# Optimization experiments

Measured on AMD Instinct MI355X. Metric: run time of the kernel, lower is better.

The kernel has to match this reference:

```python
import jax, jax.numpy as jnp
import numpy as np

B, S, D = 1, 1024, 1024
NH, DH, DR = 8, 128, 64
DCQ, DC = 768, 256
INTER, E, TOPK = 512, 8, 2

def rmsnorm(x, w, eps=1e-6):
    return x * jax.lax.rsqrt(jnp.mean(x * x, -1, keepdims=True) + eps) * w

def lin(x, w, b):
    return x @ w.T + b

def apply_rope(x, cos, sin):
    # x: [b, s, h, d]; cos/sin: [S, d//2]; complex rotate pairs (even, odd)
    b, s, h, d = x.shape
    xr = x.reshape(b, s, h, d // 2, 2)
    x0, x1 = xr[..., 0], xr[..., 1]
    c = cos[None, :s, None, :]
    sn = sin[None, :s, None, :]
    return jnp.stack([x0 * c - x1 * sn, x0 * sn + x1 * c], -1).reshape(b, s, h, d)

def setup_inputs():
    keys = iter(jax.random.split(jax.random.key(0), 64))
    def nrm(*shape):
        return jax.random.normal(next(keys), shape, jnp.float32) * 0.02
    theta = 1.0 / (10000.0 ** (jnp.arange(0, DR, 2, dtype=jnp.float32) / DR))
    ang = jnp.arange(S, dtype=jnp.float32)[:, None] * theta[None, :]
    return dict(
        h=jax.random.normal(next(keys), (B, S, D), jnp.float32),
        freqs_cos=jnp.cos(ang), freqs_sin=jnp.sin(ang),
        mask=jnp.triu(jnp.ones((S, S), bool), 1),
        attn_norm_w=jnp.ones(D), ffn_norm_w=jnp.ones(D),
        wq_down=nrm(DCQ, D), bq_down=jnp.zeros(DCQ), q_norm_w=jnp.ones(DCQ),
        wqc=nrm(NH * DH, DCQ), bqc=jnp.zeros(NH * DH),
        wqr=nrm(NH * DR, DCQ), bqr=jnp.zeros(NH * DR),
        wkr=nrm(DR, D), bkr=jnp.zeros(DR), kr_norm_w=jnp.ones(DR),
        wkv_down=nrm(DC, D), bkv_down=jnp.zeros(DC), kv_norm_w=jnp.ones(DC),
        wkc=nrm(NH * DH, DC), bkc=jnp.zeros(NH * DH),
        wvc=nrm(NH * DH, DC), bvc=jnp.zeros(NH * DH),
        wo=nrm(D, NH * DH), bo=jnp.zeros(D),
        sw1=nrm(INTER, D), sb1=jnp.zeros(INTER), sw2=nrm(D, INTER), sb2=jnp.zeros(D),
        sw3=nrm(INTER, D), sb3=jnp.zeros(INTER),
        ew1=nrm(E, INTER, D), eb1=jnp.zeros((E, INTER)), ew2=nrm(E, D, INTER), eb2=jnp.zeros((E, D)),
        ew3=nrm(E, INTER, D), eb3=jnp.zeros((E, INTER)),
        centroids=jax.random.normal(next(keys), (E, D), jnp.float32), biases=jnp.zeros(E),
    )

def _forward(h, freqs_cos, freqs_sin, mask, attn_norm_w, ffn_norm_w, wq_down, bq_down, q_norm_w, wqc, bqc, wqr, bqr, wkr, bkr, kr_norm_w, wkv_down, bkv_down, kv_norm_w, wkc, bkc, wvc, bvc, wo, bo, sw1, sb1, sw2, sb2, sw3, sb3, ew1, eb1, ew2, eb2, ew3, eb3, centroids, biases):
    b, s, _ = h.shape
    # --- pre-norm MLA attention ---
    x = rmsnorm(h, attn_norm_w)
    cQ = rmsnorm(lin(x, wq_down, bq_down), q_norm_w)
    qR = apply_rope(lin(cQ, wqr, bqr).reshape(b, s, NH, DR), freqs_cos, freqs_sin)
    qC = lin(cQ, wqc, bqc).reshape(b, s, NH, DH)
    q = jnp.concatenate([qC, qR], -1)                      # [b,s,NH,DH+DR]
    kR = apply_rope(rmsnorm(lin(x, wkr, bkr), kr_norm_w).reshape(b, s, 1, DR), freqs_cos, freqs_sin)
    cKV = rmsnorm(lin(x, wkv_down, bkv_down), kv_norm_w)
    kC = lin(cKV, wkc, bkc).reshape(b, s, NH, DH)
    vC = lin(cKV, wvc, bvc).reshape(b, s, NH, DH)
    k = jnp.concatenate([jnp.broadcast_to(kR, (b, s, NH, DR)), kC], -1)  # source order: [kR, kC]
    scores = jnp.einsum('bqhd,bkhd->bhqk', q, k) / jnp.sqrt(jnp.float32(DH + DR))
    scores = jnp.where(mask[None, None], jnp.finfo(scores.dtype).min, scores)
    attw = jax.nn.softmax(scores, -1)                      # dropout in eval mode = identity
    attn = jnp.einsum('bhqk,bkhd->bqhd', attw, vC).reshape(b, s, NH * DH)
    x1 = h + lin(attn, wo, bo)
    # --- pre-norm MoE FFN ---
    y = rmsnorm(x1, ffn_norm_w)
    shared = lin(jax.nn.silu(lin(y, sw1, sb1)) * lin(y, sw3, sb3), sw2, sb2)  # mean over 1 shared expert
    affinity = jax.nn.sigmoid(y @ centroids.T)             # [b,s,E]
    _, topi = jax.lax.top_k(affinity + biases, TOPK)
    gates = jax.nn.softmax(jnp.take_along_axis(affinity, topi, -1), -1)      # [b,s,TOPK]
    combine = (jax.nn.one_hot(topi, E, dtype=y.dtype) * gates[..., None]).sum(-2)  # [b,s,E]
    h1 = jax.nn.silu(jnp.einsum('bsd,eid->bsei', y, ew1) + eb1) * (jnp.einsum('bsd,eid->bsei', y, ew3) + eb3)
    out_e = jnp.einsum('bsei,edi->bsed', h1, ew2) + eb2
    routed = (out_e * combine[..., None]).sum(2)
    return x1 + shared + routed

def reference(h, freqs_cos, freqs_sin, mask, attn_norm_w, ffn_norm_w, wq_down, bq_down, q_norm_w, wqc, bqc, wqr, bqr, wkr, bkr, kr_norm_w, wkv_down, bkv_down, kv_norm_w, wkc, bkc, wvc, bvc, wo, bo, sw1, sb1, sw2, sb2, sw3, sb3, ew1, eb1, ew2, eb2, ew3, eb3, centroids, biases):
    return _forward(h, freqs_cos, freqs_sin, mask, attn_norm_w, ffn_norm_w, wq_down, bq_down, q_norm_w, wqc, bqc, wqr, bqr, wkr, bkr, kr_norm_w, wkv_down, bkv_down, kv_norm_w, wkc, bkc, wvc, bvc, wo, bo, sw1, sb1, sw2, sb2, sw3, sb3, ew1, eb1, ew2, eb2, ew3, eb3, centroids, biases)
```

## Files before the change

kernel.cpp:

```cpp
#include <hip/hip_runtime.h>

typedef unsigned short u16;
typedef __attribute__((ext_vector_type(8))) short short8;
typedef __attribute__((ext_vector_type(4))) float f32x4;

__device__ __forceinline__ float b2f(u16 u) { return __uint_as_float(((unsigned)u) << 16); }
__device__ __forceinline__ u16 f2b(float f) {
    unsigned x = __float_as_uint(f);
    return (u16)((x + 0x7fffu + ((x >> 16) & 1u)) >> 16);
}

#define GLDS16(gp, lp) __builtin_amdgcn_global_load_lds( \
    (const __attribute__((address_space(1))) void*)(gp), \
    (__attribute__((address_space(3))) void*)(lp), 16, 0, 0)

#define WAITV(N) do { \
    asm volatile("s_waitcnt vmcnt(" #N ")" ::: "memory"); \
    __builtin_amdgcn_sched_barrier(0); \
} while (0)

#define KC8_SWZ(lane) ((((lane) & 3) ^ (((lane) >> 3) & 3)) << 3)
#define RD_SWZ(fm, fq) (((fq) ^ (((fm) >> 1) & 3)) << 3)

__device__ __forceinline__ void xcd_swz(int& bx, int& by) {
    if ((gridDim.x & 7) == 0 && gridDim.y == 16) {
        int lid = bx + by * gridDim.x;
        int q = lid >> 3, r = lid & 7;
        by = q & 15;
        bx = r + ((q >> 4) << 3);
    }
}

struct Seg { const u16* W; const float* bias; void* C; int ldc; int epi; int bx0; int aidx; };
struct GArgs {
    const u16* A[2]; int lda[2]; int K[2];
    Seg seg[4]; int nseg;
    const float* res;
    float* dst2;
};

__launch_bounds__(256)
__global__ void mgemm4(GArgs ga)
{
    __shared__ u16 As[6 * 2048];
    __shared__ u16 Bs[6 * 2048];
    int bx = blockIdx.x, by = blockIdx.y;
    xcd_swz(bx, by);
    int si = 0;
#pragma unroll
    for (int i = 1; i < 4; i++)
        if (i < ga.nseg && bx >= ga.seg[i].bx0) si = i;
    const u16* Wp = ga.seg[si].W;
    const float* bp = ga.seg[si].bias;
    void* Cp = ga.seg[si].C;
    const int ldco = ga.seg[si].ldc;
    const int epi = ga.seg[si].epi;
    const int ai = ga.seg[si].aidx;
    const u16* Ap = ga.A[ai];
    const int lda = ga.lda[ai], K = ga.K[ai];
    const int col0 = (bx - ga.seg[si].bx0) * 64;
    const int row0 = by * 64;

    int tid = threadIdx.x;
    int lane = tid & 63, w = tid >> 6;
    int r0 = (w << 4) + (lane >> 2), kc8 = KC8_SWZ(lane);
    const u16* gA = Ap + (size_t)(row0 + r0) * lda + kc8;
    const u16* gB = Wp + (size_t)(col0 + r0) * lda + kc8;

    int fm = lane & 15, fq = lane >> 4;
    const int so = RD_SWZ(fm, fq);
    f32x4 acc[4] = {};

#define MG_STAGE(BS, KO) do { \
    GLDS16(gA + (KO), As + (BS) * 2048 + (w << 9)); \
    GLDS16(gB + (KO), Bs + (BS) * 2048 + (w << 9)); \
} while (0)

    const int nst = K >> 5;
    MG_STAGE(0, 0); MG_STAGE(1, 32); MG_STAGE(2, 64); MG_STAGE(3, 96);
    int bcur = 0;
    for (int t = 0; t < nst; t += 2) {
        if (t < nst - 2) { WAITV(4); } else { WAITV(0); }
        __builtin_amdgcn_s_barrier();
        int w4 = bcur + 4; if (w4 >= 6) w4 -= 6;
        int w5 = w4 + 1;   if (w5 >= 6) w5 -= 6;
        if (t + 4 < nst) MG_STAGE(w4, (t + 4) << 5);
        if (t + 5 < nst) MG_STAGE(w5, (t + 5) << 5);
#pragma unroll
        for (int sub = 0; sub < 2; sub++) {
            int bc = bcur + sub; if (bc >= 6) bc -= 6;
            short8 af = *(const short8*)(As + bc * 2048 + (w << 9) + fm * 32 + so);
            short8 bf[4];
#pragma unroll
            for (int nt = 0; nt < 4; nt++)
                bf[nt] = *(const short8*)(Bs + bc * 2048 + ((nt << 4) + fm) * 32 + so);
#pragma unroll
            for (int nt = 0; nt < 4; nt++)
                acc[nt] = __builtin_amdgcn_mfma_f32_16x16x32_bf16(af, bf[nt], acc[nt], 0, 0, 0);
        }
        bcur += 2; if (bcur >= 6) bcur -= 6;
    }
#undef MG_STAGE

    int rbase = row0 + (w << 4) + (fq << 2);
#pragma unroll
    for (int nt = 0; nt < 4; nt++) {
        int c = col0 + (nt << 4) + fm;
        float bcol = bp[c];
#pragma unroll
        for (int reg = 0; reg < 4; reg++) {
            int r = rbase + reg;
            float v = acc[nt][reg] + bcol;
            if (epi == 3)
                ((u16*)Cp)[(size_t)r * ldco + c] = f2b(v);
            else if (epi == 1) {
                float o = v + ga.res[(size_t)r * ldco + c];
                ((float*)Cp)[(size_t)r * ldco + c] = o;
                if (ga.dst2) ga.dst2[(size_t)r * ldco + c] = o;
            } else
                ((float*)Cp)[(size_t)r * ldco + c] = v;
        }
    }
}

__launch_bounds__(256)
__global__ void mega_glu(const u16* __restrict__ Y16,
                         const u16* __restrict__ sw1, const float* __restrict__ sb1,
                         const u16* __restrict__ sw3, const float* __restrict__ sb3,
                         const u16* __restrict__ ew1, const float* __restrict__ eb1,
                         const u16* __restrict__ ew3, const float* __restrict__ eb3,
                         u16* __restrict__ Gb,
                         const int* __restrict__ lists, const int* __restrict__ counts)
{
    __shared__ u16 As[6 * 2048];
    __shared__ u16 B1s[6 * 2048];
    __shared__ u16 B3s[6 * 2048];
    int bx = blockIdx.x, by = blockIdx.y, z = blockIdx.z;
    xcd_swz(bx, by);
    int col0 = bx * 64;
    int cnt = 1024; const int* list = nullptr;
    const u16 *W1p, *W3p; const float *b1p, *b3p;
    if (z == 0) {
        W1p = sw1; b1p = sb1; W3p = sw3; b3p = sb3;
    } else {
        int e = z - 1; cnt = counts[e]; list = lists + (e << 10);
        W1p = ew1 + (size_t)e * 512 * 1024; b1p = eb1 + e * 512;
        W3p = ew3 + (size_t)e * 512 * 1024; b3p = eb3 + e * 512;
    }
    int row0 = by * 64;
    if (row0 >= cnt) return;
    u16* Cp = Gb + (size_t)z * 524288;

    int tid = threadIdx.x, lane = tid & 63, w = tid >> 6;
    int r0 = (w << 4) + (lane >> 2), kc8 = KC8_SWZ(lane);
    int ar = row0 + r0;
    if (z > 0) ar = list[ar < cnt ? ar : cnt - 1];
    const u16* gA = Y16 + (size_t)ar * 1024 + kc8;
    const u16* gB1 = W1p + (size_t)(col0 + r0) * 1024 + kc8;
    const u16* gB3 = W3p + (size_t)(col0 + r0) * 1024 + kc8;

    int fm = lane & 15, fq = lane >> 4;
    const int so = RD_SWZ(fm, fq);
    f32x4 accU[4] = {}, accV[4] = {};

#define GL_STAGE(BS, KO) do { \
    GLDS16(gA + (KO),  As  + (BS) * 2048 + (w << 9)); \
    GLDS16(gB1 + (KO), B1s + (BS) * 2048 + (w << 9)); \
    GLDS16(gB3 + (KO), B3s + (BS) * 2048 + (w << 9)); \
} while (0)

    GL_STAGE(0, 0); GL_STAGE(1, 32); GL_STAGE(2, 64); GL_STAGE(3, 96);
    int bcur = 0;
    for (int t = 0; t < 32; t += 2) {
        if (t < 30) { WAITV(6); } else { WAITV(0); }
        __builtin_amdgcn_s_barrier();
        int w4 = bcur + 4; if (w4 >= 6) w4 -= 6;
        int w5 = w4 + 1;   if (w5 >= 6) w5 -= 6;
        if (t + 4 < 32) GL_STAGE(w4, (t + 4) << 5);
        if (t + 5 < 32) GL_STAGE(w5, (t + 5) << 5);
#pragma unroll
        for (int sub = 0; sub < 2; sub++) {
            int bc = bcur + sub; if (bc >= 6) bc -= 6;
            short8 af = *(const short8*)(As + bc * 2048 + (w << 9) + fm * 32 + so);
#pragma unroll
            for (int nt = 0; nt < 4; nt++) {
                short8 b1 = *(const short8*)(B1s + bc * 2048 + ((nt << 4) + fm) * 32 + so);
                accU[nt] = __builtin_amdgcn_mfma_f32_16x16x32_bf16(af, b1, accU[nt], 0, 0, 0);
            }
#pragma unroll
            for (int nt = 0; nt < 4; nt++) {
                short8 b3 = *(const short8*)(B3s + bc * 2048 + ((nt << 4) + fm) * 32 + so);
                accV[nt] = __builtin_amdgcn_mfma_f32_16x16x32_bf16(af, b3, accV[nt], 0, 0, 0);
            }
        }
        bcur += 2; if (bcur >= 6) bcur -= 6;
    }
#undef GL_STAGE

    int rbase = row0 + (w << 4) + (fq << 2);
#pragma unroll
    for (int nt = 0; nt < 4; nt++) {
        int c = col0 + (nt << 4) + fm;
        float b1c = b1p[c], b3c = b3p[c];
#pragma unroll
        for (int reg = 0; reg < 4; reg++) {
            int r = rbase + reg;
            if (r >= cnt) continue;
            float u = b2f(f2b(accU[nt][reg] + b1c));
            float v = b2f(f2b(accV[nt][reg] + b3c));
            Cp[(size_t)r * 512 + c] = f2b(u / (1.f + __expf(-u)) * v);
        }
    }
}

__launch_bounds__(256)
__global__ void mega_down(const u16* __restrict__ Gb,
                          const u16* __restrict__ sw2, const float* __restrict__ sb2,
                          const u16* __restrict__ ew2, const float* __restrict__ eb2,
                          float* __restrict__ Dscr,
                          const int* __restrict__ counts)
{
    __shared__ u16 Gs[6 * 2048];
    __shared__ u16 Ws[6 * 2048];
    int bx = blockIdx.x, by = blockIdx.y, z = blockIdx.z;
    xcd_swz(bx, by);
    int cnt = 1024;
    const u16* Wp; const float* bp;
    if (z == 0) { Wp = sw2; bp = sb2; }
    else {
        int e = z - 1;
        cnt = counts[e];
        Wp = ew2 + (size_t)e * 1024 * 512; bp = eb2 + e * 1024;
    }
    int row0 = by * 64;
    if (row0 >= cnt) return;
    const u16* Ap = Gb + (size_t)z * 524288;
    int col0 = bx * 64;
    float* Dp = Dscr + (size_t)z * 1048576;

    int tid = threadIdx.x, lane = tid & 63, w = tid >> 6;
    int r0 = (w << 4) + (lane >> 2), kc8 = KC8_SWZ(lane);
    const u16* gG = Ap + (size_t)(row0 + r0) * 512 + kc8;
    const u16* gW = Wp + (size_t)(col0 + r0) * 512 + kc8;

    int fm = lane & 15, fq = lane >> 4;
    const int so = RD_SWZ(fm, fq);
    f32x4 acc[4] = {};

#define MD_STAGE(BS, KO) do { \
    GLDS16(gG + (KO), Gs + (BS) * 2048 + (w << 9)); \
    GLDS16(gW + (KO), Ws + (BS) * 2048 + (w << 9)); \
} while (0)

    MD_STAGE(0, 0); MD_STAGE(1, 32); MD_STAGE(2, 64); MD_STAGE(3, 96);
    int bcur = 0;
    for (int t = 0; t < 16; t += 2) {
        if (t < 14) { WAITV(4); } else { WAITV(0); }
        __builtin_amdgcn_s_barrier();
        int w4 = bcur + 4; if (w4 >= 6) w4 -= 6;
        int w5 = w4 + 1;   if (w5 >= 6) w5 -= 6;
        if (t + 4 < 16) MD_STAGE(w4, (t + 4) << 5);
        if (t + 5 < 16) MD_STAGE(w5, (t + 5) << 5);
#pragma unroll
        for (int sub = 0; sub < 2; sub++) {
            int bc = bcur + sub; if (bc >= 6) bc -= 6;
            short8 af = *(const short8*)(Gs + bc * 2048 + (w << 9) + fm * 32 + so);
            short8 bf[4];
#pragma unroll
            for (int nt = 0; nt < 4; nt++)
                bf[nt] = *(const short8*)(Ws + bc * 2048 + ((nt << 4) + fm) * 32 + so);
#pragma unroll
            for (int nt = 0; nt < 4; nt++)
                acc[nt] = __builtin_amdgcn_mfma_f32_16x16x32_bf16(af, bf[nt], acc[nt], 0, 0, 0);
        }
        bcur += 2; if (bcur >= 6) bcur -= 6;
    }
#undef MD_STAGE

    int rbase = row0 + (w << 4) + (fq << 2);
#pragma unroll
    for (int nt = 0; nt < 4; nt++) {
        int c = col0 + (nt << 4) + fm;
        float bcol = bp[c];
#pragma unroll
        for (int reg = 0; reg < 4; reg++) {
            int r = rbase + reg;
            Dp[(size_t)r * 1024 + c] = acc[nt][reg] + bcol;
        }
    }
}

__launch_bounds__(256)
__global__ void ffn_combine(const float* __restrict__ Dscr,
                            const int* __restrict__ sE, const int* __restrict__ sP,
                            const float* __restrict__ sG,
                            float* __restrict__ out)
{
    int t = blockIdx.x, tid = threadIdx.x;
    int e0 = sE[t * 2], e1 = sE[t * 2 + 1];
    int p0 = sP[t * 2], p1 = sP[t * 2 + 1];
    float g0 = sG[t * 2], g1 = sG[t * 2 + 1];
    const float4* Ds = (const float4*)(Dscr + (size_t)t * 1024);
    const float4* D0 = (const float4*)(Dscr + (size_t)(e0 + 1) * 1048576 + (size_t)p0 * 1024);
    const float4* D1 = (const float4*)(Dscr + (size_t)(e1 + 1) * 1048576 + (size_t)p1 * 1024);
    float4* o = (float4*)(out + (size_t)t * 1024);
    float4 a = o[tid], s = Ds[tid], x0 = D0[tid], x1 = D1[tid];
    a.x += s.x + g0 * x0.x + g1 * x1.x;
    a.y += s.y + g0 * x0.y + g1 * x1.y;
    a.z += s.z + g0 * x0.z + g1 * x1.z;
    a.w += s.w + g0 * x0.w + g1 * x1.w;
    o[tid] = a;
}

__launch_bounds__(256)
__global__ void attn_mfma(const u16* __restrict__ Qp, const u16* __restrict__ Kp,
                          const u16* __restrict__ VT,
                          float* __restrict__ Opart, float* __restrict__ MLp,
                          int* __restrict__ flags, u16* __restrict__ O16)
{
    const int qt = blockIdx.x, h = blockIdx.y, z = blockIdx.z;
    const int q0 = qt * 64;
    const int tid = threadIdx.x;
    const int lane = tid & 63, w = tid >> 6;
    const int fm = lane & 15, fq = lane >> 4;

    __shared__ u16 Ks[2 * 12288];
    __shared__ u16 Vs[4 * 4096];
    __shared__ u16 Ps[4 * 2048];

    const u16* qrow = Qp + ((size_t)h * 1024 + q0 + w * 16 + fm) * 192;
    short8 qf[6];
#pragma unroll
    for (int c = 0; c < 6; c++)
        qf[c] = *(const short8*)(qrow + c * 32 + fq * 8);

    const u16* Kb = Kp + (size_t)h * 1024 * 192;
    const u16* Vb = VT + (size_t)h * 128 * 1024;

    float m_i[4], l_i[4];
#pragma unroll
    for (int r = 0; r < 4; r++) { m_i[r] = -1e30f; l_i[r] = 0.f; }
    f32x4 accO[8] = {};
    const float scale = 0.07216878364870323f;
    const int nkt = (qt >> 1) + 1;
    const int half0 = (nkt + 1) >> 1;
    const int ktlo = z ? half0 : 0;
    const int kthi = z ? nkt : half0;
    const int rbase = w * 16 + fq * 4;

    for (int kt = ktlo; kt < kthi; ++kt) {
        const int kt0 = kt * 128;
#pragma unroll
        for (int half = 0; half < 2; half++) {
            const int o = kt0 + half * 64;
#pragma unroll
            for (int i = 0; i < 6; i++) {
                int idx = w + 4 * i;
                int c = idx >> 2, k4 = idx & 3;
                const u16* g = Kb + (size_t)(o + k4 * 16 + (lane >> 2)) * 192 + c * 32 + (lane & 3) * 8;
                GLDS16(g, Ks + half * 12288 + c * 2048 + k4 * 512 + lane * 8);
            }
#pragma unroll
            for (int i = 0; i < 4; i++) {
                int idx = w + 4 * i;
                int kc = idx >> 3, k8 = idx & 7;
                const u16* g = Vb + (size_t)(k8 * 16 + (lane >> 2)) * 1024 + o + kc * 32 + (lane & 3) * 8;
                GLDS16(g, Vs + (half * 2 + kc) * 4096 + k8 * 512 + lane * 8);
            }
        }
        __syncthreads();
        f32x4 sacc[8];
        __builtin_amdgcn_s_setprio(1);
#pragma unroll
        for (int nt = 0; nt < 8; nt++) {
            sacc[nt] = (f32x4){0.f, 0.f, 0.f, 0.f};
#pragma unroll
            for (int c = 0; c < 6; c++) {
                short8 kf = *(const short8*)(Ks + (nt >> 2) * 12288 + c * 2048 + ((nt & 3) * 16 + fm) * 32 + fq * 8);
                sacc[nt] = __builtin_amdgcn_mfma_f32_16x16x32_bf16(qf[c], kf, sacc[nt], 0, 0, 0);
            }
        }
        __builtin_amdgcn_s_setprio(0);
        float pv[8][4], rmax[4];
#pragma unroll
        for (int reg = 0; reg < 4; reg++) {
            int q = q0 + rbase + reg;
            float mx = -1e30f;
#pragma unroll
            for (int nt = 0; nt < 8; nt++) {
                int gk = kt0 + nt * 16 + fm;
                float s = sacc[nt][reg] * scale;
                if (gk > q) s = -1e30f;
                pv[nt][reg] = s;
                mx = fmaxf(mx, s);
            }
            rmax[reg] = mx;
        }
#pragma unroll
        for (int m = 1; m < 16; m <<= 1)
#pragma unroll
            for (int reg = 0; reg < 4; reg++)
                rmax[reg] = fmaxf(rmax[reg], __shfl_xor(rmax[reg], m));
        float alpha[4], rsum[4];
#pragma unroll
        for (int reg = 0; reg < 4; reg++) {
            float mn = fmaxf(m_i[reg], rmax[reg]);
            alpha[reg] = __expf(m_i[reg] - mn);
            m_i[reg] = mn;
            float s = 0.f;
#pragma unroll
            for (int nt = 0; nt < 8; nt++) {
                float p = __expf(pv[nt][reg] - mn);
                pv[nt][reg] = p;
                s += p;
            }
            rsum[reg] = s;
        }
#pragma unroll
        for (int m = 1; m < 16; m <<= 1)
#pragma unroll
            for (int reg = 0; reg < 4; reg++)
                rsum[reg] += __shfl_xor(rsum[reg], m);
#pragma unroll
        for (int reg = 0; reg < 4; reg++)
            l_i[reg] = l_i[reg] * alpha[reg] + rsum[reg];
#pragma unroll
        for (int nt = 0; nt < 8; nt++)
#pragma unroll
            for (int reg = 0; reg < 4; reg++)
                Ps[w * 2048 + (nt >> 1) * 512 + (fq * 4 + reg) * 32 + (nt & 1) * 16 + fm]
                    = f2b(pv[nt][reg]);
#pragma unroll
        for (int n2 = 0; n2 < 8; n2++)
#pragma unroll
            for (int reg = 0; reg < 4; reg++)
                accO[n2][reg] *= alpha[reg];
        short8 pf[4];
#pragma unroll
        for (int kc = 0; kc < 4; kc++)
            pf[kc] = *(const short8*)(Ps + w * 2048 + kc * 512 + fm * 32 + fq * 8);
        __builtin_amdgcn_s_setprio(1);
#pragma unroll
        for (int n2 = 0; n2 < 8; n2++)
#pragma unroll
            for (int kc = 0; kc < 4; kc++) {
                short8 vf = *(const short8*)(Vs + kc * 4096 + (n2 * 16 + fm) * 32 + fq * 8);
                accO[n2] = __builtin_amdgcn_mfma_f32_16x16x32_bf16(pf[kc], vf, accO[n2], 0, 0, 0);
            }
        __builtin_amdgcn_s_setprio(0);
        __syncthreads();
    }
    float* Ob = Opart + ((size_t)(z * 8 + h) * 1024) * 128;
#pragma unroll
    for (int reg = 0; reg < 4; reg++) {
        int row = q0 + rbase + reg;
#pragma unroll
        for (int n2 = 0; n2 < 8; n2++)
            Ob[(size_t)row * 128 + n2 * 16 + fm] = accO[n2][reg];
        if (fm == 0) {
            MLp[((size_t)(z * 8 + h) * 1024 + row) * 2]     = m_i[reg];
            MLp[((size_t)(z * 8 + h) * 1024 + row) * 2 + 1] = l_i[reg];
        }
    }
    __shared__ int oldv_s;
    __threadfence();
    __syncthreads();
    if (tid == 0)
        oldv_s = __hip_atomic_fetch_add(flags + qt * 8 + h, 1,
                                        __ATOMIC_ACQ_REL, __HIP_MEMORY_SCOPE_AGENT);
    __syncthreads();
    if (oldv_s != 1) return;
    __threadfence();
    const float* O0 = Opart + ((size_t)h * 1024) * 128;
    const float* O1 = Opart + ((size_t)(8 + h) * 1024) * 128;
    for (int i = tid; i < 2048; i += 256) {
        int row = q0 + (i >> 5);
        int c4 = (i & 31) << 2;
        float m0 = MLp[((size_t)h * 1024 + row) * 2];
        float l0 = MLp[((size_t)h * 1024 + row) * 2 + 1];
        float m1 = MLp[((size_t)(8 + h) * 1024 + row) * 2];
        float l1 = MLp[((size_t)(8 + h) * 1024 + row) * 2 + 1];
        float M = fmaxf(m0, m1);
        float w0 = __expf(m0 - M), w1 = __expf(m1 - M);
        float inv = 1.f / (l0 * w0 + l1 * w1);
        float4 a = *(const float4*)(O0 + (size_t)row * 128 + c4);
        float4 b = *(const float4*)(O1 + (size_t)row * 128 + c4);
        u16* op = O16 + (size_t)row * 1024 + h * 128 + c4;
        op[0] = f2b((a.x * w0 + b.x * w1) * inv);
        op[1] = f2b((a.y * w0 + b.y * w1) * inv);
        op[2] = f2b((a.z * w0 + b.z * w1) * inv);
        op[3] = f2b((a.w * w0 + b.w * w1) * inv);
    }
}

__launch_bounds__(256)
__global__ void rmsnorm2x(const float* __restrict__ X0, const float* __restrict__ w0,
                          u16* __restrict__ O0, int c0,
                          const float* __restrict__ X1, const float* __restrict__ w1,
                          u16* __restrict__ O1, int c1)
{
    int b = blockIdx.x, tid = threadIdx.x;
    const float* X; const float* w; u16* O; int cols; int r;
    if (b < 1024) { X = X0; w = w0; O = O0; cols = c0; r = b; }
    else          { X = X1; w = w1; O = O1; cols = c1; r = b - 1024; }
    const float* xr = X + (size_t)r * cols;
    float ss = 0.f;
    for (int j = tid; j < cols; j += 256) { float v = xr[j]; ss += v * v; }
    __shared__ float red[256];
    red[tid] = ss; __syncthreads();
    for (int st = 128; st > 0; st >>= 1) { if (tid < st) red[tid] += red[tid + st]; __syncthreads(); }
    float scale = rsqrtf(red[0] / cols + 1e-6f);
    for (int j = tid; j < cols; j += 256)
        O[(size_t)r * cols + j] = f2b(xr[j] * scale * w[j]);
}

__launch_bounds__(256)
__global__ void rmsnorm_route(const float* __restrict__ X1, const float* __restrict__ ffnw,
                              u16* __restrict__ Y16,
                              const float* __restrict__ cent, const float* __restrict__ biases,
                              int* __restrict__ counts, int* __restrict__ lists,
                              int* __restrict__ sE, int* __restrict__ sP,
                              float* __restrict__ sG)
{
    __shared__ float red[256];
    int b = blockIdx.x, tid = threadIdx.x;
    if (b < 1024) {
        int r = b;
        const float* xr = X1 + (size_t)r * 1024;
        float ss = 0.f;
        for (int j = tid; j < 1024; j += 256) { float v = xr[j]; ss += v * v; }
        red[tid] = ss; __syncthreads();
        for (int st = 128; st > 0; st >>= 1) { if (tid < st) red[tid] += red[tid + st]; __syncthreads(); }
        float scale = rsqrtf(red[0] / 1024.f + 1e-6f);
        for (int j = tid; j < 1024; j += 256)
            Y16[(size_t)r * 1024 + j] = f2b(xr[j] * scale * ffnw[j]);
    } else {
        int t = b - 1024;
        const float* xr = X1 + (size_t)t * 1024;
        float ss = 0.f;
        float acc[8] = {};
        for (int j = tid; j < 1024; j += 256) {
            float x = xr[j];
            ss += x * x;
            float yp = x * ffnw[j];
#pragma unroll
            for (int e = 0; e < 8; e++) acc[e] += yp * cent[e * 1024 + j];
        }
        red[tid] = ss; __syncthreads();
        for (int st = 128; st > 0; st >>= 1) { if (tid < st) red[tid] += red[tid + st]; __syncthreads(); }
        float scale = rsqrtf(red[0] / 1024.f + 1e-6f);
        __syncthreads();
        __shared__ float aff[8];
        for (int e = 0; e < 8; e++) {
            red[tid] = acc[e]; __syncthreads();
            for (int st = 128; st > 0; st >>= 1) { if (tid < st) red[tid] += red[tid + st]; __syncthreads(); }
            if (tid == 0) aff[e] = 1.f / (1.f + expf(-red[0] * scale));
            __syncthreads();
        }
        if (tid == 0) {
            float sb[8];
#pragma unroll
            for (int e = 0; e < 8; e++) sb[e] = aff[e] + biases[e];
            int i0 = 0;
            for (int e = 1; e < 8; e++) if (sb[e] > sb[i0]) i0 = e;
            int i1 = -1;
            for (int e = 0; e < 8; e++) { if (e == i0) continue; if (i1 < 0 || sb[e] > sb[i1]) i1 = e; }
            float a0 = aff[i0], a1 = aff[i1];
            float mx = fmaxf(a0, a1);
            float e0 = expf(a0 - mx), e1 = expf(a1 - mx);
            float inv = 1.f / (e0 + e1);
            int p0 = atomicAdd(&counts[i0], 1);
            lists[i0 * 1024 + p0] = t;
            int p1 = atomicAdd(&counts[i1], 1);
            lists[i1 * 1024 + p1] = t;
            sE[t * 2] = i0; sP[t * 2] = p0; sG[t * 2] = e0 * inv;
            sE[t * 2 + 1] = i1; sP[t * 2 + 1] = p1; sG[t * 2 + 1] = e1 * inv;
        }
    }
}

__launch_bounds__(256)
__global__ void pack_all(const float* __restrict__ QC, const float* __restrict__ QRr,
                         const float* __restrict__ KRraw, const float* __restrict__ krw,
                         const float* __restrict__ KC,
                         const u16* __restrict__ VCb,
                         const float* __restrict__ fcos, const float* __restrict__ fsin,
                         u16* __restrict__ Qp, u16* __restrict__ Kp, u16* __restrict__ VT)
{
    __shared__ u16 Ts[64][68];
    __shared__ float kshared[64];
    int b = blockIdx.x, tid = threadIdx.x;
    if (b < 1024) {
        int s = b;
        if (tid < 64) {
            float v = KRraw[(size_t)s * 64 + tid];
            float ss = v * v;
#pragma unroll
            for (int m = 1; m < 64; m <<= 1) ss += __shfl_xor(ss, m);
            float scale = rsqrtf(ss / 64.f + 1e-6f);
            int j = tid >> 1;
            float c = fcos[s * 32 + j], sn = fsin[s * 32 + j];
            float x0 = KRraw[(size_t)s * 64 + (tid & ~1)] * scale * krw[tid & ~1];
            float x1 = KRraw[(size_t)s * 64 + (tid | 1)]  * scale * krw[tid | 1];
            kshared[tid] = (tid & 1) ? (x0 * sn + x1 * c) : (x0 * c - x1 * sn);
        }
        __syncthreads();
        for (int e = tid; e < 1536; e += 256) {
            int h = e / 192, d = e % 192;
            float q;
            if (d < 128) {
                q = QC[(size_t)s * 1024 + h * 128 + d];
            } else {
                int dd = d - 128, j = dd >> 1;
                float c = fcos[s * 32 + j], sn = fsin[s * 32 + j];
                float x0 = QRr[(size_t)s * 512 + h * 64 + (dd & ~1)];
                float x1 = QRr[(size_t)s * 512 + h * 64 + (dd | 1)];
                q = (dd & 1) ? (x0 * sn + x1 * c) : (x0 * c - x1 * sn);
            }
            Qp[((size_t)h * 1024 + s) * 192 + d] = f2b(q);
            float k = (d < 64) ? kshared[d]
                               : KC[(size_t)s * 1024 + h * 128 + d - 64];
            Kp[((size_t)h * 1024 + s) * 192 + d] = f2b(k);
        }
    } else {
        int idx = b - 1024;
        int s0 = (idx & 15) * 64, d0 = (idx >> 4) * 64;
        for (int k = 0; k < 16; k++) {
            int e = tid + k * 256, r = e >> 6, c = e & 63;
            Ts[r][c] = VCb[(size_t)(s0 + r) * 1024 + d0 + c];
        }
        __syncthreads();
        for (int k = 0; k < 16; k++) {
            int e = tid + k * 256, d = e >> 6, s = e & 63;
            VT[(size_t)(d0 + d) * 1024 + s0 + s] = Ts[s][d];
        }
    }
}

#define NCAST 4096
__launch_bounds__(256)
__global__ void fused_cast(const float* p0, const float* p1, const float* p2,
                           const float* p3, const float* p4, const float* p5,
                           const float* p6, const float* p7, const float* p8,
                           const float* p9, const float* p10, const float* p11,
                           const float* p12, const float* pkr,
                           u16* __restrict__ dst,
                           const float* __restrict__ hX, const float* __restrict__ attnw,
                           u16* __restrict__ X16, int* __restrict__ zc)
{
    __shared__ float red[256];
    int b = blockIdx.x, tid = threadIdx.x;
    if (b < NCAST) {
        const int NQ = 18022400 / 4;
        for (int i = b * 256 + tid; i < NQ; i += NCAST * 256) {
            int e = i * 4;
            const float* s; int base;
            if      (e <   786432) { s = p0;  base = 0; }
            else if (e <  1048576) { s = p1;  base =   786432; }
            else if (e <  1835008) { s = p2;  base =  1048576; }
            else if (e <  2228224) { s = p3;  base =  1835008; }
            else if (e <  2490368) { s = p4;  base =  2228224; }
            else if (e <  2752512) { s = p5;  base =  2490368; }
            else if (e <  3801088) { s = p6;  base =  2752512; }
            else if (e <  4325376) { s = p7;  base =  3801088; }
            else if (e <  4849664) { s = p8;  base =  4325376; }
            else if (e <  5373952) { s = p9;  base =  4849664; }
            else if (e <  9568256) { s = p10; base =  5373952; }
            else if (e < 13762560) { s = p11; base =  9568256; }
            else if (e < 17956864) { s = p12; base = 13762560; }
            else                   { s = pkr; base = 17956864; }
            float4 v = *(const float4*)(s + (e - base));
            ushort4 o;
            o.x = f2b(v.x); o.y = f2b(v.y); o.z = f2b(v.z); o.w = f2b(v.w);
            *(ushort4*)(dst + e) = o;
        }
    } else {
        int r = b - NCAST;
        if (r == 0 && tid < 136) zc[tid] = 0;
        const float* xr = hX + (size_t)r * 1024;
        float ss = 0.f;
        for (int j = tid; j < 1024; j += 256) { float v = xr[j]; ss += v * v; }
        red[tid] = ss; __syncthreads();
        for (int st = 128; st > 0; st >>= 1) { if (tid < st) red[tid] += red[tid + st]; __syncthreads(); }
        float scale = rsqrtf(red[0] / 1024.f + 1e-6f);
        for (int j = tid; j < 1024; j += 256)
            X16[(size_t)r * 1024 + j] = f2b(xr[j] * scale * attnw[j]);
    }
}

extern "C" void kernel_launch(void* const* d_in, const int* in_sizes, int n_in,
                              void* d_out, int out_size, void* d_ws, size_t ws_size,
                              hipStream_t stream)
{
    (void)in_sizes; (void)n_in; (void)ws_size; (void)out_size;
    const float* h       = (const float*)d_in[0];
    const float* fcos    = (const float*)d_in[1];
    const float* fsin    = (const float*)d_in[2];
    const float* attn_w  = (const float*)d_in[4];
    const float* ffn_w   = (const float*)d_in[5];
    const float* wq_down = (const float*)d_in[6];
    const float* bq_down = (const float*)d_in[7];
    const float* q_norm  = (const float*)d_in[8];
    const float* wqc     = (const float*)d_in[9];
    const float* bqc     = (const float*)d_in[10];
    const float* wqr     = (const float*)d_in[11];
    const float* bqr     = (const float*)d_in[12];
    const float* wkr     = (const float*)d_in[13];
    const float* bkr     = (const float*)d_in[14];
    const float* kr_norm = (const float*)d_in[15];
    const float* wkv     = (const float*)d_in[16];
    const float* bkv     = (const float*)d_in[17];
    const float* kv_norm = (const float*)d_in[18];
    const float* wkc     = (const float*)d_in[19];
    const float* bkc     = (const float*)d_in[20];
    const float* wvc     = (const float*)d_in[21];
    const float* bvc     = (const float*)d_in[22];
    const float* wo      = (const float*)d_in[23];
    const float* bo      = (const float*)d_in[24];
    const float* sw1     = (const float*)d_in[25];
    const float* sb1     = (const float*)d_in[26];
    const float* sw2     = (const float*)d_in[27];
    const float* sb2     = (const float*)d_in[28];
    const float* sw3     = (const float*)d_in[29];
    const float* sb3     = (const float*)d_in[30];
    const float* ew1     = (const float*)d_in[31];
    const float* eb1     = (const float*)d_in[32];
    const float* ew2     = (const float*)d_in[33];
    const float* eb2     = (const float*)d_in[34];
    const float* ew3     = (const float*)d_in[35];
    const float* eb3     = (const float*)d_in[36];
    const float* cent    = (const float*)d_in[37];
    const float* biases  = (const float*)d_in[38];

    char* wsb = (char*)d_ws;
    const size_t U5 = 512 * 1024;
    u16*   X16   = (u16*)(wsb + 8 * U5);
    float* QRr   = (float*)(wsb + 12 * U5);
    float* CQraw = (float*)(wsb + 16 * U5);
    u16*   ATT16 = (u16*)(wsb + 16 * U5);
    u16*   CQ16  = (u16*)(wsb + 22 * U5);
    float* CKVraw= (float*)(wsb + 25 * U5);
    u16*   CKV16 = (u16*)(wsb + 27 * U5);
    float* KRraw = (float*)(wsb + 28 * U5);
    float* QC    = (float*)(wsb + 29 * U5);
    float* KC    = (float*)(wsb + 37 * U5);
    float* X1    = (float*)(wsb + 53 * U5);
    int*   counts= (int*)(wsb + 61 * U5 + 64 * 1024);
    int*   flags = counts + 8;
    int*   lists = (int*)(wsb + 61 * U5 + 32 * 1024);
    int*   sE    = (int*)(wsb + 61 * U5 + 72 * 1024);
    int*   sP    = (int*)(wsb + 61 * U5 + 80 * 1024);
    float* sG    = (float*)(wsb + 61 * U5 + 88 * 1024);
    u16*   Y16   = (u16*)(wsb + 69 * U5);
    u16*   Gb    = (u16*)(wsb + 73 * U5);

    u16* wb = (u16*)(wsb + 92 * U5);
    u16 *c_wq  = wb;
    u16 *c_wkv = c_wq  + 786432;
    u16 *c_wqc = c_wkv + 262144;
    u16 *c_wqr = c_wqc + 786432;
    u16 *c_wkc = c_wqr + 393216;
    u16 *c_wvc = c_wkc + 262144;
    u16 *c_wo  = c_wvc + 262144;
    u16 *c_sw1 = c_wo  + 1048576;
    u16 *c_sw3 = c_sw1 + 524288;
    u16 *c_sw2 = c_sw3 + 524288;
    u16 *c_ew1 = c_sw2 + 524288;
    u16 *c_ew3 = c_ew1 + 4194304;
    u16 *c_ew2 = c_ew3 + 4194304;
    u16 *c_wkr = c_ew2 + 4194304;
    u16* VCb = (u16*)(wsb + 92 * U5 + 36175872);
    u16* VTp = VCb + 1048576;
    u16* Qpk = VTp + 1048576;
    u16* Kpk = Qpk + 1572864;
    float* Opart = (float*)(wsb + 192 * U5);
    float* MLp   = (float*)(wsb + 209 * U5);
    float* Dscr  = (float*)(wsb + 224 * U5);

    fused_cast<<<NCAST + 1024, 256, 0, stream>>>(wq_down, wkv, wqc, wqr, wkc, wvc, wo,
                                                 sw1, sw3, sw2, ew1, ew3, ew2, wkr, wb,
                                                 h, attn_w, X16, counts);

    {
        GArgs g = {};
        g.A[0] = X16; g.lda[0] = 1024; g.K[0] = 1024;
        g.seg[0] = { c_wq,  bq_down, CQraw,  768, 0, 0,  0 };
        g.seg[1] = { c_wkv, bkv,     CKVraw, 256, 0, 12, 0 };
        g.seg[2] = { c_wkr, bkr,     KRraw,  64,  0, 16, 0 };
        g.nseg = 3;
        mgemm4<<<dim3(17, 16), 256, 0, stream>>>(g);
    }
    rmsnorm2x<<<2048, 256, 0, stream>>>(CQraw, q_norm, CQ16, 768,
                                        CKVraw, kv_norm, CKV16, 256);
    {
        GArgs g = {};
        g.A[0] = CQ16;  g.lda[0] = 768; g.K[0] = 768;
        g.A[1] = CKV16; g.lda[1] = 256; g.K[1] = 256;
        g.seg[0] = { c_wqc, bqc, QC,   1024, 0, 0,  0 };
        g.seg[1] = { c_wqr, bqr, QRr,  512,  0, 16, 0 };
        g.seg[2] = { c_wkc, bkc, KC,   1024, 0, 24, 1 };
        g.seg[3] = { c_wvc, bvc, VCb,  1024, 3, 40, 1 };
        g.nseg = 4;
        mgemm4<<<dim3(56, 16), 256, 0, stream>>>(g);
    }
    pack_all<<<1280, 256, 0, stream>>>(QC, QRr, KRraw, kr_norm, KC, VCb, fcos, fsin,
                                       Qpk, Kpk, VTp);
    attn_mfma<<<dim3(16, 8, 2), 256, 0, stream>>>(Qpk, Kpk, VTp, Opart, MLp,
                                                  flags, ATT16);
    {
        GArgs g = {};
        g.A[0] = ATT16; g.lda[0] = 1024; g.K[0] = 1024;
        g.seg[0] = { c_wo, bo, X1, 1024, 1, 0, 0 };
        g.nseg = 1; g.res = h; g.dst2 = (float*)d_out;
        mgemm4<<<dim3(16, 16), 256, 0, stream>>>(g);
    }

    rmsnorm_route<<<2048, 256, 0, stream>>>(X1, ffn_w, Y16, cent, biases,
                                            counts, lists, sE, sP, sG);
    mega_glu<<<dim3(8, 16, 9), 256, 0, stream>>>(Y16, c_sw1, sb1, c_sw3, sb3,
                                                 c_ew1, eb1, c_ew3, eb3,
                                                 Gb, lists, counts);
    mega_down<<<dim3(16, 16, 9), 256, 0, stream>>>(Gb, c_sw2, sb2, c_ew2, eb2,
                                                   Dscr, counts);
    ffn_combine<<<1024, 256, 0, stream>>>(Dscr, sE, sP, sG, (float*)d_out);
}
```

Measured before the change: 387.6 us.

## Split causal attention four ways over 64-key tiles with separate combine kernel

The attention kernel now processes 64-key tiles instead of 128-key tiles and splits each query tile's causal key range across four blocks instead of two, doubling the grid. The in-kernel combine, which used an atomic flag so the last-arriving block merged the partial results, is replaced by a standalone attn_combine4 kernel that merges the four partial outputs using their running max and sum. The aim is to cut masked work on the diagonal, improve occupancy and load balance, and drop the atomic and fence path. In exchange it adds a kernel launch and more traffic for partial outputs, and some splits for early query tiles end up empty.

New measurement: 341.8 us, median of 2. -11.8%, faster.

```diff
diff --git a/kernel.cpp b/kernel.cpp
--- a/kernel.cpp
+++ b/kernel.cpp
@@ -315,8 +315,7 @@
 __launch_bounds__(256)
 __global__ void attn_mfma(const u16* __restrict__ Qp, const u16* __restrict__ Kp,
                           const u16* __restrict__ VT,
-                          float* __restrict__ Opart, float* __restrict__ MLp,
-                          int* __restrict__ flags, u16* __restrict__ O16)
+                          float* __restrict__ Opart, float* __restrict__ MLp)
 {
     const int qt = blockIdx.x, h = blockIdx.y, z = blockIdx.z;
     const int q0 = qt * 64;
@@ -324,9 +323,9 @@
     const int lane = tid & 63, w = tid >> 6;
     const int fm = lane & 15, fq = lane >> 4;
 
-    __shared__ u16 Ks[2 * 12288];
-    __shared__ u16 Vs[4 * 4096];
-    __shared__ u16 Ps[4 * 2048];
+    __shared__ u16 Ks[12288];
+    __shared__ u16 Vs[8192];
+    __shared__ u16 Ps[4096];
 
     const u16* qrow = Qp + ((size_t)h * 1024 + q0 + w * 16 + fm) * 192;
     short8 qf[6];
@@ -342,53 +341,48 @@
     for (int r = 0; r < 4; r++) { m_i[r] = -1e30f; l_i[r] = 0.f; }
     f32x4 accO[8] = {};
     const float scale = 0.07216878364870323f;
-    const int nkt = (qt >> 1) + 1;
-    const int half0 = (nkt + 1) >> 1;
-    const int ktlo = z ? half0 : 0;
-    const int kthi = z ? nkt : half0;
+    const int nt64 = qt + 1;
+    const int ktlo = (z * nt64) >> 2;
+    const int kthi = ((z + 1) * nt64) >> 2;
     const int rbase = w * 16 + fq * 4;
 
     for (int kt = ktlo; kt < kthi; ++kt) {
-        const int kt0 = kt * 128;
-#pragma unroll
-        for (int half = 0; half < 2; half++) {
-            const int o = kt0 + half * 64;
-#pragma unroll
-            for (int i = 0; i < 6; i++) {
-                int idx = w + 4 * i;
-                int c = idx >> 2, k4 = idx & 3;
-                const u16* g = Kb + (size_t)(o + k4 * 16 + (lane >> 2)) * 192 + c * 32 + (lane & 3) * 8;
-                GLDS16(g, Ks + half * 12288 + c * 2048 + k4 * 512 + lane * 8);
-            }
-#pragma unroll
-            for (int i = 0; i < 4; i++) {
-                int idx = w + 4 * i;
-                int kc = idx >> 3, k8 = idx & 7;
-                const u16* g = Vb + (size_t)(k8 * 16 + (lane >> 2)) * 1024 + o + kc * 32 + (lane & 3) * 8;
-                GLDS16(g, Vs + (half * 2 + kc) * 4096 + k8 * 512 + lane * 8);
-            }
+        const int o = kt * 64;
+#pragma unroll
+        for (int i = 0; i < 6; i++) {
+            int idx = w + 4 * i;
+            int c = idx >> 2, k4 = idx & 3;
+            const u16* g = Kb + (size_t)(o + k4 * 16 + (lane >> 2)) * 192 + c * 32 + (lane & 3) * 8;
+            GLDS16(g, Ks + c * 2048 + k4 * 512 + lane * 8);
+        }
+#pragma unroll
+        for (int i = 0; i < 4; i++) {
+            int idx = w + 4 * i;
+            int kc = idx >> 3, k8 = idx & 7;
+            const u16* g = Vb + (size_t)(k8 * 16 + (lane >> 2)) * 1024 + o + kc * 32 + (lane & 3) * 8;
+            GLDS16(g, Vs + kc * 4096 + k8 * 512 + lane * 8);
         }
         __syncthreads();
-        f32x4 sacc[8];
+        f32x4 sacc[4];
         __builtin_amdgcn_s_setprio(1);
 #pragma unroll
-        for (int nt = 0; nt < 8; nt++) {
+        for (int nt = 0; nt < 4; nt++) {
             sacc[nt] = (f32x4){0.f, 0.f, 0.f, 0.f};
 #pragma unroll
             for (int c = 0; c < 6; c++) {
-                short8 kf = *(const short8*)(Ks + (nt >> 2) * 12288 + c * 2048 + ((nt & 3) * 16 + fm) * 32 + fq * 8);
+                short8 kf = *(const short8*)(Ks + c * 2048 + (nt * 16 + fm) * 32 + fq * 8);
                 sacc[nt] = __builtin_amdgcn_mfma_f32_16x16x32_bf16(qf[c], kf, sacc[nt], 0, 0, 0);
             }
         }
         __builtin_amdgcn_s_setprio(0);
-        float pv[8][4], rmax[4];
+        float pv[4][4], rmax[4];
 #pragma unroll
         for (int reg = 0; reg < 4; reg++) {
             int q = q0 + rbase + reg;
             float mx = -1e30f;
 #pragma unroll
-            for (int nt = 0; nt < 8; nt++) {
-                int gk = kt0 + nt * 16 + fm;
+            for (int nt = 0; nt < 4; nt++) {
+                int gk = o + nt * 16 + fm;
                 float s = sacc[nt][reg] * scale;
                 if (gk > q) s = -1e30f;
                 pv[nt][reg] = s;
@@ -409,7 +403,7 @@
             m_i[reg] = mn;
             float s = 0.f;
 #pragma unroll
-            for (int nt = 0; nt < 8; nt++) {
+            for (int nt = 0; nt < 4; nt++) {
                 float p = __expf(pv[nt][reg] - mn);
                 pv[nt][reg] = p;
                 s += p;
@@ -425,25 +419,25 @@
         for (int reg = 0; reg < 4; reg++)
             l_i[reg] = l_i[reg] * alpha[reg] + rsum[reg];
 #pragma unroll
-        for (int nt = 0; nt < 8; nt++)
+        for (int nt = 0; nt < 4; nt++)
 #pragma unroll
             for (int reg = 0; reg < 4; reg++)
-                Ps[w * 2048 + (nt >> 1) * 512 + (fq * 4 + reg) * 32 + (nt & 1) * 16 + fm]
+                Ps[w * 1024 + (nt >> 1) * 512 + (fq * 4 + reg) * 32 + (nt & 1) * 16 + fm]
                     = f2b(pv[nt][reg]);
 #pragma unroll
         for (int n2 = 0; n2 < 8; n2++)
 #pragma unroll
             for (int reg = 0; reg < 4; reg++)
                 accO[n2][reg] *= alpha[reg];
-        short8 pf[4];
-#pragma unroll
-        for (int kc = 0; kc < 4; kc++)
-            pf[kc] = *(const short8*)(Ps + w * 2048 + kc * 512 + fm * 32 + fq * 8);
+        short8 pf[2];
+#pragma unroll
+        for (int kc = 0; kc < 2; kc++)
+            pf[kc] = *(const short8*)(Ps + w * 1024 + kc * 512 + fm * 32 + fq * 8);
         __builtin_amdgcn_s_setprio(1);
 #pragma unroll
         for (int n2 = 0; n2 < 8; n2++)
 #pragma unroll
-            for (int kc = 0; kc < 4; kc++) {
+            for (int kc = 0; kc < 2; kc++) {
                 short8 vf = *(const short8*)(Vs + kc * 4096 + (n2 * 16 + fm) * 32 + fq * 8);
                 accO[n2] = __builtin_amdgcn_mfma_f32_16x16x32_bf16(pf[kc], vf, accO[n2], 0, 0, 0);
             }
@@ -462,34 +456,36 @@
             MLp[((size_t)(z * 8 + h) * 1024 + row) * 2 + 1] = l_i[reg];
         }
     }
-    __shared__ int oldv_s;
-    __threadfence();
-    __syncthreads();
-    if (tid == 0)
-        oldv_s = __hip_atomic_fetch_add(flags + qt * 8 + h, 1,
-                                        __ATOMIC_ACQ_REL, __HIP_MEMORY_SCOPE_AGENT);
-    __syncthreads();
-    if (oldv_s != 1) return;
-    __threadfence();
-    const float* O0 = Opart + ((size_t)h * 1024) * 128;
-    const float* O1 = Opart + ((size_t)(8 + h) * 1024) * 128;
-    for (int i = tid; i < 2048; i += 256) {
-        int row = q0 + (i >> 5);
-        int c4 = (i & 31) << 2;
-        float m0 = MLp[((size_t)h * 1024 + row) * 2];
-        float l0 = MLp[((size_t)h * 1024 + row) * 2 + 1];
-        float m1 = MLp[((size_t)(8 + h) * 1024 + row) * 2];
-        float l1 = MLp[((size_t)(8 + h) * 1024 + row) * 2 + 1];
-        float M = fmaxf(m0, m1);
-        float w0 = __expf(m0 - M), w1 = __expf(m1 - M);
-        float inv = 1.f / (l0 * w0 + l1 * w1);
-        float4 a = *(const float4*)(O0 + (size_t)row * 128 + c4);
-        float4 b = *(const float4*)(O1 + (size_t)row * 128 + c4);
-        u16* op = O16 + (size_t)row * 1024 + h * 128 + c4;
-        op[0] = f2b((a.x * w0 + b.x * w1) * inv);
-        op[1] = f2b((a.y * w0 + b.y * w1) * inv);
-        op[2] = f2b((a.z * w0 + b.z * w1) * inv);
-        op[3] = f2b((a.w * w0 + b.w * w1) * inv);
+}
+
+__launch_bounds__(256)
+__global__ void attn_combine4(const float* __restrict__ Opart,
+                              const float* __restrict__ MLp,
+                              u16* __restrict__ O)
+{
+    int tid = threadIdx.x;
+    int rowg = blockIdx.x * 16 + (tid >> 4);
+    int h = rowg >> 10, row = rowg & 1023;
+    int c0 = (tid & 15) * 8;
+    float m[4], l[4];
+    float M = -1e30f;
+#pragma unroll
+    for (int z = 0; z < 4; z++) {
+        m[z] = MLp[((size_t)(z * 8 + h) * 1024 + row) * 2];
+        l[z] = MLp[((size_t)(z * 8 + h) * 1024 + row) * 2 + 1];
+        M = fmaxf(M, m[z]);
+    }
+    float wz[4], den = 0.f;
+#pragma unroll
+    for (int z = 0; z < 4; z++) { wz[z] = __expf(m[z] - M); den += l[z] * wz[z]; }
+    float inv = 1.f / den;
+#pragma unroll
+    for (int j = 0; j < 8; j++) {
+        float o = 0.f;
+#pragma unroll
+        for (int z = 0; z < 4; z++)
+            o += Opart[((size_t)(z * 8 + h) * 1024 + row) * 128 + c0 + j] * wz[z];
+        O[(size_t)row * 1024 + h * 128 + c0 + j] = f2b(o * inv);
     }
 }
 
@@ -676,7 +672,7 @@
         }
     } else {
         int r = b - NCAST;
-        if (r == 0 && tid < 136) zc[tid] = 0;
+        if (r == 0 && tid < 8) zc[tid] = 0;
         const float* xr = hX + (size_t)r * 1024;
         float ss = 0.f;
         for (int j = tid; j < 1024; j += 256) { float v = xr[j]; ss += v * v; }
@@ -746,7 +742,6 @@
     float* KC    = (float*)(wsb + 37 * U5);
     float* X1    = (float*)(wsb + 53 * U5);
     int*   counts= (int*)(wsb + 61 * U5 + 64 * 1024);
-    int*   flags = counts + 8;
     int*   lists = (int*)(wsb + 61 * U5 + 32 * 1024);
     int*   sE    = (int*)(wsb + 61 * U5 + 72 * 1024);
     int*   sP    = (int*)(wsb + 61 * U5 + 80 * 1024);
@@ -774,8 +769,8 @@
     u16* Qpk = VTp + 1048576;
     u16* Kpk = Qpk + 1572864;
     float* Opart = (float*)(wsb + 192 * U5);
-    float* MLp   = (float*)(wsb + 209 * U5);
     float* Dscr  = (float*)(wsb + 224 * U5);
+    float* MLp   = (float*)(wsb + 296 * U5);
 
     fused_cast<<<NCAST + 1024, 256, 0, stream>>>(wq_down, wkv, wqc, wqr, wkc, wvc, wo,
                                                  sw1, sw3, sw2, ew1, ew3, ew2, wkr, wb,
@@ -805,8 +800,8 @@
     }
     pack_all<<<1280, 256, 0, stream>>>(QC, QRr, KRraw, kr_norm, KC, VCb, fcos, fsin,
                                        Qpk, Kpk, VTp);
-    attn_mfma<<<dim3(16, 8, 2), 256, 0, stream>>>(Qpk, Kpk, VTp, Opart, MLp,
-                                                  flags, ATT16);
+    attn_mfma<<<dim3(16, 8, 4), 256, 0, stream>>>(Qpk, Kpk, VTp, Opart, MLp);
+    attn_combine4<<<512, 256, 0, stream>>>(Opart, MLp, ATT16);
     {
         GArgs g = {};
         g.A[0] = ATT16; g.lda[0] = 1024; g.K[0] = 1024;
```
